# Kernel tuning notes

Measured on AMD Instinct MI355X. Metric: run time of the kernel, lower is better.

Reference implementation:

```python
import jax, jax.numpy as jnp
import numpy as np

IN_DIM = 128
OUT_DIM = 128
EDGE_DIM = 64
NUM_HEADS = 8
HEAD_DIM = OUT_DIM // NUM_HEADS
N_NODES = 10000
N_EDGES = 320000
LN_EPS = 1e-5


def _gelu(x):
    # torch nn.GELU default is the exact (erf) formulation
    return jax.nn.gelu(x, approximate=False)


def _layernorm(x, g, b):
    mu = jnp.mean(x, axis=-1, keepdims=True)
    var = jnp.var(x, axis=-1, keepdims=True)
    return (x - mu) * jax.lax.rsqrt(var + LN_EPS) * g + b


def setup_inputs() -> dict:
    key = jax.random.key(0)
    ks = jax.random.split(key, 16)

    def lin(k, fan_in, fan_out):
        # torch nn.Linear default init: U(-1/sqrt(fan_in), 1/sqrt(fan_in))
        bound = 1.0 / np.sqrt(fan_in)
        kw, kb = jax.random.split(k)
        w = jax.random.uniform(kw, (fan_in, fan_out), jnp.float32, -bound, bound)
        b = jax.random.uniform(kb, (fan_out,), jnp.float32, -bound, bound)
        return w, b

    node_features = jax.random.normal(ks[0], (N_NODES, IN_DIM), jnp.float32)
    edge_index = jax.random.randint(ks[1], (2, N_EDGES), 0, N_NODES)
    edge_attr = jax.random.normal(ks[2], (N_EDGES, EDGE_DIM), jnp.float32)

    msg_w1, msg_b1 = lin(ks[3], 2 * IN_DIM + EDGE_DIM, OUT_DIM)
    msg_w2, msg_b2 = lin(ks[4], OUT_DIM, OUT_DIM)
    q_w, q_b = lin(ks[5], IN_DIM, OUT_DIM)
    kv_w, kv_b = lin(ks[6], IN_DIM + EDGE_DIM, OUT_DIM)
    out_w1, out_b1 = lin(ks[7], IN_DIM + OUT_DIM, OUT_DIM)
    out_w2, out_b2 = lin(ks[8], OUT_DIM, OUT_DIM)
    ln_g = 1.0 + 0.02 * jax.random.normal(ks[9], (OUT_DIM,), jnp.float32)
    ln_b = 0.02 * jax.random.normal(ks[10], (OUT_DIM,), jnp.float32)

    return dict(node_features=node_features, edge_attr=edge_attr,
                msg_w1=msg_w1, msg_b1=msg_b1, msg_w2=msg_w2, msg_b2=msg_b2,
                q_w=q_w, q_b=q_b, kv_w=kv_w, kv_b=kv_b,
                out_w1=out_w1, out_b1=out_b1, out_w2=out_w2, out_b2=out_b2,
                ln_g=ln_g, ln_b=ln_b, edge_index=edge_index)


def reference(node_features, edge_attr, msg_w1, msg_b1, msg_w2, msg_b2,
              q_w, q_b, kv_w, kv_b, out_w1, out_b1, out_w2, out_b2,
              ln_g, ln_b, edge_index):
    N = node_features.shape[0]
    E = edge_index.shape[1]
    src, dst = edge_index[0], edge_index[1]

    s = node_features[src]                      # [E, Din]
    d = node_features[dst]                      # [E, Din]

    # message MLP
    m_in = jnp.concatenate([s, d, edge_attr], axis=-1)          # [E, 2*Din+De]
    m = _gelu(m_in @ msg_w1 + msg_b1) @ msg_w2 + msg_b2         # [E, Dout]

    # per-edge attention logits
    q = (d @ q_w + q_b).reshape(E, NUM_HEADS, HEAD_DIM)
    kv_in = jnp.concatenate([s, edge_attr], axis=-1)
    kv = (kv_in @ kv_w + kv_b).reshape(E, NUM_HEADS, HEAD_DIM)
    attn = jnp.sum(q * kv, axis=-1) * (HEAD_DIM ** -0.5)        # [E, H]

    # Deterministic version: pick the edge with the largest index per dst node.
    last = jnp.full((N,), -1, dtype=jnp.int32).at[dst].max(
        jnp.arange(E, dtype=jnp.int32))                          # [N]
    attn_full = jnp.where(last[:, None] >= 0,
                          attn[jnp.maximum(last, 0)],
                          -jnp.inf)                              # [N, H]
    # softmax over the NODE axis (dim=0), exactly as the torch code does;
    # -inf rows contribute 0, so using N instead of dst.max()+1 is identical.
    attn_norm = jax.nn.softmax(attn_full, axis=0)[dst]           # [E, H]

    m = (m.reshape(E, NUM_HEADS, HEAD_DIM) * attn_norm[..., None]).reshape(E, OUT_DIM)

    # scatter-add aggregation
    agg = jax.ops.segment_sum(m, dst, num_segments=N)            # [N, Dout]

    h_in = jnp.concatenate([node_features, agg], axis=-1)        # [N, Din+Dout]
    h = _gelu(h_in @ out_w1 + out_b1) @ out_w2 + out_b2          # [N, Dout]

    # res_proj is Identity since in_dim == out_dim; dropout is eval-mode no-op
    return _layernorm(node_features + h, ln_g, ln_b)
```

## Files before the change

### kernel.cpp

```cpp
#include <hip/hip_runtime.h>
#include <hip/hip_bf16.h>

#define NN 10000
#define NE 320000

typedef __bf16 bf16x8 __attribute__((ext_vector_type(8)));
typedef float  f32x4  __attribute__((ext_vector_type(4)));

__device__ __forceinline__ float bf2f(ushort u){
  union { uint i; float f; } c; c.i = ((uint)u) << 16; return c.f;
}
__device__ __forceinline__ ushort f2bf(float f){
  union { float f; uint i; } c; c.f = f;
  uint x = c.i;
  return (ushort)((x + 0x7FFFu + ((x >> 16) & 1u)) >> 16);
}
__device__ __forceinline__ float gelu_erf(float x){
  return 0.5f * x * (1.0f + erff(x * 0.70710678118654752f));
}
__device__ __forceinline__ float gelu_tanh(float x){
  float y = 0.7978845608028654f * (x + 0.044715f * x * x * x);
  float e = __expf(2.f * y);
  float th = 1.f - 2.f / (e + 1.f);
  return 0.5f * x * (1.f + th);
}
__device__ __forceinline__ uint encf(float f){
  uint u = __float_as_uint(f);
  return (u & 0x80000000u) ? ~u : (u | 0x80000000u);
}
__device__ __forceinline__ float decf(uint u){
  return __uint_as_float((u & 0x80000000u) ? (u & 0x7FFFFFFFu) : ~u);
}
#define MFMA16(a,b,c) __builtin_amdgcn_mfma_f32_16x16x32_bf16((a),(b),(c),0,0,0)

__global__ void k_init(const uint* __restrict__ w, int* __restrict__ flag,
                       int* __restrict__ cnt, int* __restrict__ last,
                       uint* __restrict__ Menc, float* __restrict__ S){
  int t = threadIdx.x;
  if (blockIdx.x == 0){
    uint c = 0;
    for (int i = t; i < 4096; i += 256){
      uint v = w[i * 63];
      uint e = (v >> 7) & 0xFF;
      if (e >= 100 && e <= 140) c++;
    }
    __shared__ uint red[256];
    red[t] = c; __syncthreads();
    for (int s = 128; s > 0; s >>= 1){
      if (t < s) red[t] += red[t + s];
      __syncthreads();
    }
    if (t == 0) *flag = (red[0] < 2048) ? 1 : 0;
    return;
  }
  int idx = (blockIdx.x - 1) * 256 + t;
  if (idx < 10000) last[idx] = -1;
  else if (idx < 20000) cnt[idx - 10000] = 0;
  else if (idx < 20008) Menc[idx - 20000] = 0u;
  else if (idx < 20016) S[idx - 20008] = 0.f;
}

__global__ void k_prep(
    const void* NF0, const int* __restrict__ dstI,
    const void* w1, const void* w2, const void* qw, const void* kvw,
    const void* ow1, const void* ow2,
    const void* b1, const void* b2, const void* qb, const void* kvb,
    const void* ob1, const void* ob2, const void* lg, const void* lb,
    int* __restrict__ cnt, int* __restrict__ last,
    ushort* NFc, float* Gagg, ushort* SB, ushort* KVW2,
    ushort* W1aT, ushort* W1bT, ushort* W1cT, ushort* W2T, ushort* QT, ushort* KVT,
    ushort* O1aT, ushort* O1bT, ushort* O2T, const int* flag)
{
  int f = *flag;
  int idx = blockIdx.x * 256 + threadIdx.x;
  if (idx < NE){
    int d = dstI[idx];
    atomicAdd(&cnt[d], 1);
    atomicMax(&last[d], idx);
    return;
  }
  idx -= NE;
  if (idx < 320000){
    if (f){
      float4 v = ((const float4*)NF0)[idx];
      ushort4 o; o.x=f2bf(v.x); o.y=f2bf(v.y); o.z=f2bf(v.z); o.w=f2bf(v.w);
      ((ushort4*)NFc)[idx] = o;
    } else ((ushort4*)NFc)[idx] = ((const ushort4*)NF0)[idx];
    return;
  }
  idx -= 320000;
  if (idx < 320000){ float4 z = {0.f,0.f,0.f,0.f}; ((float4*)Gagg)[idx] = z; return; }
  idx -= 320000;
  if (idx < 1024){
    const void* ps[8] = {b1,b2,qb,kvb,ob1,ob2,lg,lb};
    const void* p = ps[idx >> 7]; int j = idx & 127;
    SB[idx] = f ? f2bf(((const float*)p)[j]) : ((const ushort*)p)[j];
    return;
  }
  idx -= 1024;
  if (idx < 8192){
    KVW2[idx] = f ? f2bf(((const float*)kvw)[16384 + idx]) : ((const ushort*)kvw)[16384 + idx];
    return;
  }
  idx -= 8192;
  if (idx < 16384){ int c=idx>>7,k=idx&127; W1aT[idx] = f? f2bf(((const float*)w1)[k*128+c]) : ((const ushort*)w1)[k*128+c]; return; }
  idx -= 16384;
  if (idx < 16384){ int c=idx>>7,k=idx&127; W1bT[idx] = f? f2bf(((const float*)w1)[(128+k)*128+c]) : ((const ushort*)w1)[(128+k)*128+c]; return; }
  idx -= 16384;
  if (idx < 8192){ int c=idx>>6,k=idx&63;  W1cT[idx] = f? f2bf(((const float*)w1)[(256+k)*128+c]) : ((const ushort*)w1)[(256+k)*128+c]; return; }
  idx -= 8192;
  if (idx < 16384){ int c=idx>>7,k=idx&127; W2T[idx] = f? f2bf(((const float*)w2)[k*128+c]) : ((const ushort*)w2)[k*128+c]; return; }
  idx -= 16384;
  if (idx < 16384){ int c=idx>>7,k=idx&127; QT[idx]  = f? f2bf(((const float*)qw)[k*128+c]) : ((const ushort*)qw)[k*128+c]; return; }
  idx -= 16384;
  if (idx < 16384){ int c=idx>>7,k=idx&127; KVT[idx] = f? f2bf(((const float*)kvw)[k*128+c]) : ((const ushort*)kvw)[k*128+c]; return; }
  idx -= 16384;
  if (idx < 16384){ int c=idx>>7,k=idx&127; O1aT[idx] = f? f2bf(((const float*)ow1)[k*128+c]) : ((const ushort*)ow1)[k*128+c]; return; }
  idx -= 16384;
  if (idx < 16384){ int c=idx>>7,k=idx&127; O1bT[idx] = f? f2bf(((const float*)ow1)[(128+k)*128+c]) : ((const ushort*)ow1)[(128+k)*128+c]; return; }
  idx -= 16384;
  if (idx < 16384){ int c=idx>>7,k=idx&127; O2T[idx] = f? f2bf(((const float*)ow2)[k*128+c]) : ((const ushort*)ow2)[k*128+c]; return; }
}

__global__ __launch_bounds__(1024) void k_scan(const int* __restrict__ cnt,
                                               int* __restrict__ fill){
  __shared__ int sc[1024];
  int t = threadIdx.x;
  int base = t * 10;
  int v[10]; int tot = 0;
  #pragma unroll
  for (int j = 0; j < 10; ++j){
    int idx = base + j;
    v[j] = (idx < NN) ? cnt[idx] : 0;
    tot += v[j];
  }
  sc[t] = tot; __syncthreads();
  for (int off = 1; off < 1024; off <<= 1){
    int x = (t >= off) ? sc[t - off] : 0;
    __syncthreads();
    sc[t] += x;
    __syncthreads();
  }
  int run = sc[t] - tot;
  #pragma unroll
  for (int j = 0; j < 10; ++j){
    int idx = base + j;
    if (idx < NN) fill[idx] = run;
    run += v[j];
  }
}

__global__ __launch_bounds__(256) void k_fillperm(
    const int* __restrict__ srcI, const int* __restrict__ dstI,
    int* __restrict__ fill, int* __restrict__ sSort, int* __restrict__ dSort,
    const float* __restrict__ EAf, const ushort* __restrict__ EAb,
    ushort* __restrict__ EAs,
    const ushort* __restrict__ NFc,
    const ushort* __restrict__ W1aT, const ushort* __restrict__ W1bT,
    const ushort* __restrict__ QT,  const ushort* __restrict__ KVT,
    const ushort* __restrict__ SB,
    ushort* __restrict__ PA, ushort* __restrict__ PB,
    ushort* __restrict__ Qb, ushort* __restrict__ KV1,
    const int* __restrict__ flag)
{
  int t = threadIdx.x;
  if (blockIdx.x >= 1250){
    int l = t & 63, w = t >> 6;
    int m = l & 15, g = l >> 4;
    int row0 = ((int)blockIdx.x - 1250) * 16;
    const ushort* WT = (w==0) ? W1aT : (w==1) ? W1bT : (w==2) ? QT : KVT;
    ushort*       OUT= (w==0) ? PA   : (w==1) ? PB   : (w==2) ? Qb : KV1;
    const f32x4 FZ = {0.f,0.f,0.f,0.f};
    f32x4 acc[8];
    #pragma unroll
    for (int i = 0; i < 8; ++i) acc[i] = FZ;
    int arow = row0 + m;
    #pragma unroll
    for (int ks = 0; ks < 4; ++ks){
      int koff = ks * 32 + g * 8;
      bf16x8 a = *reinterpret_cast<const bf16x8*>(NFc + (size_t)arow * 128 + koff);
      #pragma unroll
      for (int nt = 0; nt < 8; ++nt){
        bf16x8 b = *reinterpret_cast<const bf16x8*>(WT + (size_t)(nt*16+m) * 128 + koff);
        acc[nt] = MFMA16(a, b, acc[nt]);
      }
    }
    #pragma unroll
    for (int nt = 0; nt < 8; ++nt){
      int col = nt * 16 + m;
      float bb = (w==1) ? bf2f(SB[col]) : (w==2) ? bf2f(SB[256+col]) : (w==3) ? bf2f(SB[384+col]) : 0.f;
      #pragma unroll
      for (int r = 0; r < 4; ++r){
        int row = row0 + g * 4 + r;
        OUT[(size_t)row * 128 + col] = f2bf(acc[nt][r] + bb);
      }
    }
    return;
  }
  __shared__ int sp[256];
  int e0 = blockIdx.x * 256;
  int e = e0 + t;
  {
    int d = dstI[e];
    int p = atomicAdd(&fill[d], 1);
    sSort[p] = srcI[e];
    dSort[p] = d;
    sp[t] = p;
  }
  __syncthreads();
  if (*flag){
    #pragma unroll
    for (int pass = 0; pass < 16; ++pass){
      int i = pass * 256 + t;
      int rloc = i >> 4, q = i & 15;
      int p = sp[rloc];
      float4 v = *reinterpret_cast<const float4*>(EAf + (size_t)(e0 + rloc) * 64 + q * 4);
      ushort4 o; o.x=f2bf(v.x); o.y=f2bf(v.y); o.z=f2bf(v.z); o.w=f2bf(v.w);
      *reinterpret_cast<ushort4*>(EAs + (size_t)p * 64 + q * 4) = o;
    }
  } else {
    #pragma unroll
    for (int pass = 0; pass < 8; ++pass){
      int i = pass * 256 + t;
      int rloc = i >> 3, q = i & 7;
      int p = sp[rloc];
      *reinterpret_cast<bf16x8*>(EAs + (size_t)p * 64 + q * 8) =
        *reinterpret_cast<const bf16x8*>(EAb + (size_t)(e0 + rloc) * 64 + q * 8);
    }
  }
}

__global__ __launch_bounds__(256) void k_edgeattn(
    const ushort* __restrict__ PA, const ushort* __restrict__ PB,
    const ushort* __restrict__ EAs,
    const int* __restrict__ sSort, const int* __restrict__ dSort,
    const ushort* __restrict__ W1cT,
    float* __restrict__ Gagg,
    const ushort* __restrict__ Qb, const ushort* __restrict__ KV1,
    const ushort* __restrict__ EAb, const float* __restrict__ EAf,
    const ushort* __restrict__ KVW2,
    const int* __restrict__ srcI, const int* __restrict__ last,
    float* __restrict__ attn, uint* __restrict__ Menc, const int* __restrict__ flag)
{
  __shared__ int sIdx[128], dIdx[128];
  __shared__ __align__(16) char Hs[128 * 256];
  __shared__ float ea_s[16][64];
  __shared__ int eN[16], sN[16];
  __shared__ uint lmax[8];
  int t = threadIdx.x;

  if (blockIdx.x >= 2500){
    int n0 = ((int)blockIdx.x - 2500) * 16;
    if (t < 16){
      int e = last[n0 + t];
      eN[t] = e;
      sN[t] = (e >= 0) ? srcI[e] : 0;
    }
    if (t < 8) lmax[t] = 0u;
    __syncthreads();
    int F = *flag;
    for (int i = t; i < 1024; i += 256){
      int nn = i >> 6, k = i & 63;
      int e = eN[nn];
      int ee = (e >= 0) ? e : 0;
      float v = F ? EAf[(size_t)ee * 64 + k] : bf2f(EAb[(size_t)ee * 64 + k]);
      ea_s[nn][k] = (e >= 0) ? v : 0.0f;
    }
    __syncthreads();
    int j = t & 127;
    int half = t >> 7;
    float acc[8];
    #pragma unroll
    for (int i = 0; i < 8; ++i) acc[i] = 0.f;
    for (int k = 0; k < 64; ++k){
      float wv = bf2f(KVW2[(size_t)k * 128 + j]);
      #pragma unroll
      for (int nn = 0; nn < 8; ++nn) acc[nn] += ea_s[half * 8 + nn][k] * wv;
    }
    #pragma unroll
    for (int nn = 0; nn < 8; ++nn){
      int nl = half * 8 + nn;
      int n = n0 + nl;
      int e = eN[nl];
      float kvv = acc[nn] + bf2f(KV1[(size_t)sN[nl] * 128 + j]);
      float qv  = bf2f(Qb[(size_t)n * 128 + j]);
      float p = qv * kvv;
      p += __shfl_xor(p, 1); p += __shfl_xor(p, 2);
      p += __shfl_xor(p, 4); p += __shfl_xor(p, 8);
      if ((j & 15) == 0 && e >= 0){
        float v = p * 0.25f;
        attn[(size_t)n * 8 + (j >> 4)] = v;
        atomicMax(&lmax[j >> 4], encf(v));
      }
    }
    __syncthreads();
    if (t < 8 && lmax[t]) atomicMax(&Menc[t], lmax[t]);
    return;
  }

  int p0 = blockIdx.x * 128;
  int l = t & 63, w = t >> 6;
  int rw = w >> 1, cw = w & 1;
  int m = l & 15, g = l >> 4;

  if (t < 128){ sIdx[t] = sSort[p0 + t]; dIdx[t] = dSort[p0 + t]; }
  __syncthreads();

  {
    int r = t >> 1, half = t & 1;
    int sr = sIdx[r], dr = dIdx[r];
    #pragma unroll
    for (int j = 0; j < 8; ++j){
      int c8 = half * 8 + j;
      bf16x8 pa = *reinterpret_cast<const bf16x8*>(PA + (size_t)sr * 128 + c8 * 8);
      bf16x8 pb = *reinterpret_cast<const bf16x8*>(PB + (size_t)dr * 128 + c8 * 8);
      bf16x8 ps;
      #pragma unroll
      for (int k = 0; k < 8; ++k) ps[k] = (__bf16)((float)pa[k] + (float)pb[k]);
      int byte = (r * 256 + c8 * 16) ^ ((r & 7) << 4);
      *reinterpret_cast<bf16x8*>(&Hs[byte]) = ps;
    }
  }

  const f32x4 FZ = {0.f,0.f,0.f,0.f};
  f32x4 acc[4][4];
  #pragma unroll
  for (int i = 0; i < 4; ++i)
    #pragma unroll
    for (int j = 0; j < 4; ++j) acc[i][j] = FZ;

  #pragma unroll
  for (int ks = 0; ks < 2; ++ks){
    bf16x8 af[4], bfr[4];
    #pragma unroll
    for (int rt = 0; rt < 4; ++rt){
      int rl = rw * 64 + rt * 16 + m;
      af[rt] = *reinterpret_cast<const bf16x8*>(EAs + (size_t)(p0 + rl) * 64 + ks * 32 + g * 8);
    }
    #pragma unroll
    for (int ct = 0; ct < 4; ++ct){
      int col = cw * 64 + ct * 16 + m;
      bfr[ct] = *reinterpret_cast<const bf16x8*>(W1cT + (size_t)col * 64 + ks * 32 + g * 8);
    }
    #pragma unroll
    for (int rt = 0; rt < 4; ++rt)
      #pragma unroll
      for (int ct = 0; ct < 4; ++ct)
        acc[rt][ct] = MFMA16(af[rt], bfr[ct], acc[rt][ct]);
  }
  __syncthreads();

  #pragma unroll
  for (int ct = 0; ct < 4; ++ct){
    int col = cw * 64 + ct * 16 + m;
    #pragma unroll
    for (int rt = 0; rt < 4; ++rt)
      #pragma unroll
      for (int r = 0; r < 4; ++r){
        int row = rw * 64 + rt * 16 + g * 4 + r;
        int byte = (row * 256 + col * 2) ^ ((row & 7) << 4);
        float v = gelu_tanh(acc[rt][ct][r] + bf2f(*reinterpret_cast<const ushort*>(&Hs[byte])));
        *reinterpret_cast<ushort*>(&Hs[byte]) = f2bf(v);
      }
  }
  __syncthreads();

  {
    int c = t & 127, hh = t >> 7;
    int rS = hh * 64, rE = rS + 64;
    float run = 0.f;
    int cur = dIdx[rS];
    for (int r = rS; r < rE; ++r){
      int d = dIdx[r];
      if (d != cur){
        unsafeAtomicAdd(&Gagg[(size_t)cur * 128 + c], run);
        run = 0.f; cur = d;
      }
      int byte = (r * 256 + c * 2) ^ ((r & 7) << 4);
      run += bf2f(*reinterpret_cast<const ushort*>(&Hs[byte]));
    }
    unsafeAtomicAdd(&Gagg[(size_t)cur * 128 + c], run);
  }
}

__global__ __launch_bounds__(256) void k_asum(
    const float* __restrict__ attn, const int* __restrict__ last,
    const uint* __restrict__ Menc, float* __restrict__ S)
{
  __shared__ float red[256][8];
  int t = threadIdx.x;
  float M[8];
  #pragma unroll
  for (int h = 0; h < 8; ++h) M[h] = decf(Menc[h]);
  float p[8];
  #pragma unroll
  for (int h = 0; h < 8; ++h) p[h] = 0.f;
  for (int n = blockIdx.x * 256 + t; n < NN; n += gridDim.x * 256){
    if (last[n] >= 0){
      #pragma unroll
      for (int h = 0; h < 8; ++h) p[h] += __expf(attn[(size_t)n * 8 + h] - M[h]);
    }
  }
  #pragma unroll
  for (int h = 0; h < 8; ++h) red[t][h] = p[h];
  __syncthreads();
  for (int s = 128; s > 0; s >>= 1){
    if (t < s){
      #pragma unroll
      for (int h = 0; h < 8; ++h) red[t][h] += red[t + s][h];
    }
    __syncthreads();
  }
  if (t < 8) atomicAdd(&S[t], red[0][t]);
}

__global__ __launch_bounds__(256) void k_aggmm2(
    const float* __restrict__ Gagg, const ushort* __restrict__ W2T,
    const ushort* __restrict__ O1aT, const ushort* __restrict__ O1bT,
    const ushort* __restrict__ SB,
    const int* __restrict__ cnt, const int* __restrict__ last,
    const float* __restrict__ attn, const uint* __restrict__ Menc,
    const float* __restrict__ S,
    const ushort* __restrict__ NFc, ushort* __restrict__ T1)
{
  __shared__ __align__(16) char Zs[64 * 256];
  int t = threadIdx.x, l = t & 63, w = t >> 6;
  int m = l & 15, g = l >> 4;
  int row0 = blockIdx.x * 64 + w * 16;

  float M[8], Sinv[8];
  #pragma unroll
  for (int h = 0; h < 8; ++h){ M[h] = decf(Menc[h]); Sinv[h] = 1.0f / S[h]; }

  int arow = row0 + m; if (arow >= NN) arow = NN - 1;
  const f32x4 FZ = {0.f,0.f,0.f,0.f};
  f32x4 acc[8];
  #pragma unroll
  for (int i = 0; i < 8; ++i) acc[i] = FZ;

  #pragma unroll
  for (int ks = 0; ks < 4; ++ks){
    const float* gp = Gagg + (size_t)arow * 128 + ks * 32 + g * 8;
    float4 u0 = *reinterpret_cast<const float4*>(gp);
    float4 u1 = *reinterpret_cast<const float4*>(gp + 4);
    float gv[8] = {u0.x,u0.y,u0.z,u0.w,u1.x,u1.y,u1.z,u1.w};
    bf16x8 hi, lo;
    #pragma unroll
    for (int k = 0; k < 8; ++k){
      hi[k] = (__bf16)gv[k];
      lo[k] = (__bf16)(gv[k] - (float)hi[k]);
    }
    #pragma unroll
    for (int nt = 0; nt < 8; ++nt){
      bf16x8 b = *reinterpret_cast<const bf16x8*>(W2T + (size_t)(nt*16+m) * 128 + ks * 32 + g * 8);
      acc[nt] = MFMA16(hi, b, acc[nt]);
      acc[nt] = MFMA16(lo, b, acc[nt]);
    }
  }

  #pragma unroll
  for (int r = 0; r < 4; ++r){
    int row = row0 + g * 4 + r;
    int rr = (row < NN) ? row : NN - 1;
    float cn = (float)cnt[rr];
    int lst = last[rr];
    int Lr = w * 16 + g * 4 + r;
    #pragma unroll
    for (int nt = 0; nt < 8; ++nt){
      int col = nt * 16 + m;
      float aw = (lst >= 0) ? __expf(attn[(size_t)rr * 8 + nt] - M[nt]) * Sinv[nt] : 0.f;
      float z = (acc[nt][r] + cn * bf2f(SB[128 + col])) * aw;
      int byte = (Lr * 256 + col * 2) ^ ((Lr & 7) << 4);
      *reinterpret_cast<ushort*>(&Zs[byte]) = f2bf(z);
    }
  }
  __syncthreads();

  f32x4 acc2[8];
  #pragma unroll
  for (int i = 0; i < 8; ++i) acc2[i] = FZ;
  int La = w * 16 + m;
  #pragma unroll
  for (int ks = 0; ks < 4; ++ks){
    int koff = ks * 32 + g * 8;
    bf16x8 az = *reinterpret_cast<const bf16x8*>(&Zs[(La * 256 + koff * 2) ^ ((La & 7) << 4)]);
    bf16x8 an = *reinterpret_cast<const bf16x8*>(NFc + (size_t)arow * 128 + koff);
    #pragma unroll
    for (int nt = 0; nt < 8; ++nt){
      bf16x8 b1v = *reinterpret_cast<const bf16x8*>(O1bT + (size_t)(nt*16+m) * 128 + koff);
      bf16x8 b2v = *reinterpret_cast<const bf16x8*>(O1aT + (size_t)(nt*16+m) * 128 + koff);
      acc2[nt] = MFMA16(az, b1v, acc2[nt]);
      acc2[nt] = MFMA16(an, b2v, acc2[nt]);
    }
  }
  #pragma unroll
  for (int nt = 0; nt < 8; ++nt){
    int col = nt * 16 + m;
    float bb = bf2f(SB[512 + col]);
    #pragma unroll
    for (int r = 0; r < 4; ++r){
      int row = row0 + g * 4 + r;
      if (row < NN){
        float v = gelu_erf(acc2[nt][r] + bb);
        T1[(size_t)row * 128 + col] = f2bf(v);
      }
    }
  }
}

__global__ __launch_bounds__(256) void k_out2ln(
    const ushort* __restrict__ T1, const ushort* __restrict__ O2T,
    const ushort* __restrict__ SB,
    const ushort* __restrict__ NFc, void* __restrict__ out,
    const int* __restrict__ flag)
{
  int t = threadIdx.x, l = t & 63, w = t >> 6;
  int m = l & 15, g = l >> 4;
  int row0 = blockIdx.x * 64 + w * 16;
  int F = *flag;
  int arow = row0 + m; if (arow >= NN) arow = NN - 1;
  const f32x4 FZ = {0.f,0.f,0.f,0.f};
  f32x4 acc[8];
  #pragma unroll
  for (int i = 0; i < 8; ++i) acc[i] = FZ;
  #pragma unroll
  for (int ks = 0; ks < 4; ++ks){
    int koff = ks * 32 + g * 8;
    bf16x8 a = *reinterpret_cast<const bf16x8*>(T1 + (size_t)arow * 128 + koff);
    #pragma unroll
    for (int nt = 0; nt < 8; ++nt){
      bf16x8 b = *reinterpret_cast<const bf16x8*>(O2T + (size_t)(nt*16+m) * 128 + koff);
      acc[nt] = MFMA16(a, b, acc[nt]);
    }
  }
  #pragma unroll
  for (int r = 0; r < 4; ++r){
    int row = row0 + g * 4 + r;
    bool ok = row < NN;
    int rr = ok ? row : NN - 1;
    float x[8]; float s = 0.f, q = 0.f;
    #pragma unroll
    for (int nt = 0; nt < 8; ++nt){
      int col = nt * 16 + m;
      float xv = acc[nt][r] + bf2f(SB[640 + col]) + bf2f(NFc[(size_t)rr * 128 + col]);
      x[nt] = xv; s += xv; q += xv * xv;
    }
    #pragma unroll
    for (int msk = 1; msk < 16; msk <<= 1){
      s += __shfl_xor(s, msk);
      q += __shfl_xor(q, msk);
    }
    float mean = s * (1.0f / 128.0f);
    float var  = q * (1.0f / 128.0f) - mean * mean;
    float rs = rsqrtf(var + 1e-5f);
    if (ok){
      #pragma unroll
      for (int nt = 0; nt < 8; ++nt){
        int col = nt * 16 + m;
        float y = (x[nt] - mean) * rs * bf2f(SB[768 + col]) + bf2f(SB[896 + col]);
        if (F) ((float*)out)[(size_t)row * 128 + col] = y;
        else   ((ushort*)out)[(size_t)row * 128 + col] = f2bf(y);
      }
    }
  }
}

extern "C" void kernel_launch(void* const* d_in, const int* in_sizes, int n_in,
                              void* d_out, int out_size, void* d_ws, size_t ws_size,
                              hipStream_t stream)
{
  const void* NF0  = d_in[0];
  const void* EA0  = d_in[1];
  const void* w1   = d_in[2];
  const void* b1   = d_in[3];
  const void* w2   = d_in[4];
  const void* b2   = d_in[5];
  const void* qw   = d_in[6];
  const void* qb   = d_in[7];
  const void* kvw  = d_in[8];
  const void* kvb  = d_in[9];
  const void* ow1  = d_in[10];
  const void* ob1  = d_in[11];
  const void* ow2  = d_in[12];
  const void* ob2  = d_in[13];
  const void* lg   = d_in[14];
  const void* lb   = d_in[15];
  const int*  srcI = (const int*)d_in[16];
  const int*  dstI = srcI + NE;

  char* ws = (char*)d_ws;
  size_t off = 0;
  auto alloc = [&](size_t bytes) -> void* {
    void* p = ws + off;
    off = (off + bytes + 255) & ~(size_t)255;
    return p;
  };
  int*    flag  = (int*)   alloc(4);
  ushort* NFc   = (ushort*)alloc((size_t)NN * 128 * 2);
  ushort* SB    = (ushort*)alloc(8 * 128 * 2);
  ushort* KVW2  = (ushort*)alloc(64 * 128 * 2);
  ushort* W1aT  = (ushort*)alloc(128 * 128 * 2);
  ushort* W1bT  = (ushort*)alloc(128 * 128 * 2);
  ushort* W1cT  = (ushort*)alloc(128 * 64 * 2);
  ushort* W2T   = (ushort*)alloc(128 * 128 * 2);
  ushort* QT    = (ushort*)alloc(128 * 128 * 2);
  ushort* KVT   = (ushort*)alloc(128 * 128 * 2);
  ushort* O1aT  = (ushort*)alloc(128 * 128 * 2);
  ushort* O1bT  = (ushort*)alloc(128 * 128 * 2);
  ushort* O2T   = (ushort*)alloc(128 * 128 * 2);
  int*    last  = (int*)   alloc(NN * 4);
  int*    cnt   = (int*)   alloc(NN * 4);
  int*    fill  = (int*)   alloc(NN * 4);
  int*    sSort = (int*)   alloc((size_t)NE * 4);
  int*    dSort = (int*)   alloc((size_t)NE * 4);
  ushort* EAs   = (ushort*)alloc((size_t)NE * 64 * 2);
  float*  attn  = (float*) alloc(NN * 8 * 4);
  uint*   Menc  = (uint*)  alloc(8 * 4);
  float*  S     = (float*) alloc(8 * 4);
  ushort* PA    = (ushort*)alloc((size_t)NN * 128 * 2);
  ushort* PB    = (ushort*)alloc((size_t)NN * 128 * 2);
  ushort* Qb    = (ushort*)alloc((size_t)NN * 128 * 2);
  ushort* KV1   = (ushort*)alloc((size_t)NN * 128 * 2);
  float*  Gagg  = (float*) alloc((size_t)NN * 128 * 4);
  ushort* T1    = (ushort*)alloc((size_t)NN * 128 * 2);

  k_init<<<80, 256, 0, stream>>>((const uint*)NF0, flag, cnt, last, Menc, S);
  k_prep<<<4330, 256, 0, stream>>>(NF0, dstI, w1, w2, qw, kvw, ow1, ow2,
                                   b1, b2, qb, kvb, ob1, ob2, lg, lb,
                                   cnt, last, NFc, Gagg, SB, KVW2,
                                   W1aT, W1bT, W1cT, W2T, QT, KVT, O1aT, O1bT, O2T, flag);
  k_scan<<<1, 1024, 0, stream>>>(cnt, fill);
  k_fillperm<<<1875, 256, 0, stream>>>(srcI, dstI, fill, sSort, dSort,
                                       (const float*)EA0, (const ushort*)EA0, EAs,
                                       NFc, W1aT, W1bT, QT, KVT, SB,
                                       PA, PB, Qb, KV1, flag);
  k_edgeattn<<<3125, 256, 0, stream>>>(PA, PB, EAs, sSort, dSort, W1cT, Gagg,
                                       Qb, KV1, (const ushort*)EA0, (const float*)EA0,
                                       KVW2, srcI, last, attn, Menc, flag);
  k_asum<<<40, 256, 0, stream>>>(attn, last, Menc, S);
  k_aggmm2<<<157, 256, 0, stream>>>(Gagg, W2T, O1aT, O1bT, SB, cnt, last,
                                    attn, Menc, S, NFc, T1);
  k_out2ln<<<157, 256, 0, stream>>>(T1, O2T, SB, NFc, d_out, flag);
}
```

Before: 210.1 us.

## Halve edge tile to 64 rows and replace tanh GELU with erf LUT

The edge-message kernel now handles 64 sorted edges per block instead of 128, with each wave owning 16 rows across all 8 column tiles. LDS per block shrinks and the block count doubles, which should raise occupancy and parallelism. The tanh-approximate GELU is replaced by a per-block 1025-entry LUT of exact erf GELU with linear interpolation. Each block pays to build the LUT, the smaller tiles reload the W1c fragments more often and cause more atomics to Gagg, and the interpolation only approximates exact GELU.

```diff
diff --git a/kernel.cpp b/kernel.cpp
--- a/kernel.cpp
+++ b/kernel.cpp
@@ -17,12 +17,6 @@
 }
 __device__ __forceinline__ float gelu_erf(float x){
   return 0.5f * x * (1.0f + erff(x * 0.70710678118654752f));
-}
-__device__ __forceinline__ float gelu_tanh(float x){
-  float y = 0.7978845608028654f * (x + 0.044715f * x * x * x);
-  float e = __expf(2.f * y);
-  float th = 1.f - 2.f / (e + 1.f);
-  return 0.5f * x * (1.f + th);
 }
 __device__ __forceinline__ uint encf(float f){
   uint u = __float_as_uint(f);
@@ -242,15 +236,16 @@
     const int* __restrict__ srcI, const int* __restrict__ last,
     float* __restrict__ attn, uint* __restrict__ Menc, const int* __restrict__ flag)
 {
-  __shared__ int sIdx[128], dIdx[128];
-  __shared__ __align__(16) char Hs[128 * 256];
-  __shared__ float ea_s[16][64];
+  __shared__ __align__(16) char Hs[64 * 256];
+  __shared__ float LUT[1026];
+  __shared__ int sIdx[64], dIdx[64];
   __shared__ int eN[16], sN[16];
   __shared__ uint lmax[8];
   int t = threadIdx.x;
 
-  if (blockIdx.x >= 2500){
-    int n0 = ((int)blockIdx.x - 2500) * 16;
+  if (blockIdx.x >= 5000){
+    float (*ea_s)[64] = reinterpret_cast<float(*)[64]>(Hs);
+    int n0 = ((int)blockIdx.x - 5000) * 16;
     if (t < 16){
       int e = last[n0 + t];
       eN[t] = e;
@@ -298,20 +293,20 @@
     return;
   }
 
-  int p0 = blockIdx.x * 128;
+  int p0 = blockIdx.x * 64;
   int l = t & 63, w = t >> 6;
-  int rw = w >> 1, cw = w & 1;
   int m = l & 15, g = l >> 4;
 
-  if (t < 128){ sIdx[t] = sSort[p0 + t]; dIdx[t] = dSort[p0 + t]; }
+  if (t < 64){ sIdx[t] = sSort[p0 + t]; dIdx[t] = dSort[p0 + t]; }
+  for (int i = t; i < 1025; i += 256) LUT[i] = gelu_erf((float)i * (1.0f/64.0f) - 8.0f);
   __syncthreads();
 
   {
-    int r = t >> 1, half = t & 1;
+    int r = t >> 2, q = t & 3;
     int sr = sIdx[r], dr = dIdx[r];
     #pragma unroll
-    for (int j = 0; j < 8; ++j){
-      int c8 = half * 8 + j;
+    for (int j = 0; j < 4; ++j){
+      int c8 = q * 4 + j;
       bf16x8 pa = *reinterpret_cast<const bf16x8*>(PA + (size_t)sr * 128 + c8 * 8);
       bf16x8 pb = *reinterpret_cast<const bf16x8*>(PB + (size_t)dr * 128 + c8 * 8);
       bf16x8 ps;
@@ -323,51 +318,43 @@
   }
 
   const f32x4 FZ = {0.f,0.f,0.f,0.f};
-  f32x4 acc[4][4];
-  #pragma unroll
-  for (int i = 0; i < 4; ++i)
-    #pragma unroll
-    for (int j = 0; j < 4; ++j) acc[i][j] = FZ;
+  f32x4 acc[8];
+  #pragma unroll
+  for (int i = 0; i < 8; ++i) acc[i] = FZ;
 
   #pragma unroll
   for (int ks = 0; ks < 2; ++ks){
-    bf16x8 af[4], bfr[4];
-    #pragma unroll
-    for (int rt = 0; rt < 4; ++rt){
-      int rl = rw * 64 + rt * 16 + m;
-      af[rt] = *reinterpret_cast<const bf16x8*>(EAs + (size_t)(p0 + rl) * 64 + ks * 32 + g * 8);
-    }
-    #pragma unroll
-    for (int ct = 0; ct < 4; ++ct){
-      int col = cw * 64 + ct * 16 + m;
-      bfr[ct] = *reinterpret_cast<const bf16x8*>(W1cT + (size_t)col * 64 + ks * 32 + g * 8);
-    }
-    #pragma unroll
-    for (int rt = 0; rt < 4; ++rt)
-      #pragma unroll
-      for (int ct = 0; ct < 4; ++ct)
-        acc[rt][ct] = MFMA16(af[rt], bfr[ct], acc[rt][ct]);
+    bf16x8 af = *reinterpret_cast<const bf16x8*>(EAs + (size_t)(p0 + w * 16 + m) * 64 + ks * 32 + g * 8);
+    #pragma unroll
+    for (int nt = 0; nt < 8; ++nt){
+      bf16x8 b = *reinterpret_cast<const bf16x8*>(W1cT + (size_t)(nt * 16 + m) * 64 + ks * 32 + g * 8);
+      acc[nt] = MFMA16(af, b, acc[nt]);
+    }
   }
   __syncthreads();
 
   #pragma unroll
-  for (int ct = 0; ct < 4; ++ct){
-    int col = cw * 64 + ct * 16 + m;
-    #pragma unroll
-    for (int rt = 0; rt < 4; ++rt)
-      #pragma unroll
-      for (int r = 0; r < 4; ++r){
-        int row = rw * 64 + rt * 16 + g * 4 + r;
-        int byte = (row * 256 + col * 2) ^ ((row & 7) << 4);
-        float v = gelu_tanh(acc[rt][ct][r] + bf2f(*reinterpret_cast<const ushort*>(&Hs[byte])));
-        *reinterpret_cast<ushort*>(&Hs[byte]) = f2bf(v);
-      }
+  for (int nt = 0; nt < 8; ++nt){
+    int col = nt * 16 + m;
+    #pragma unroll
+    for (int r = 0; r < 4; ++r){
+      int row = w * 16 + g * 4 + r;
+      int byte = (row * 256 + col * 2) ^ ((row & 7) << 4);
+      float x = acc[nt][r] + bf2f(*reinterpret_cast<const ushort*>(&Hs[byte]));
+      float idxf = fminf(fmaxf((x + 8.0f) * 64.0f, 0.0f), 1023.0f);
+      int i = (int)idxf;
+      float fr = idxf - (float)i;
+      float y = LUT[i] + fr * (LUT[i + 1] - LUT[i]);
+      y = (x > 7.9f) ? x : y;
+      y = (x < -7.9f) ? 0.0f : y;
+      *reinterpret_cast<ushort*>(&Hs[byte]) = f2bf(y);
+    }
   }
   __syncthreads();
 
   {
     int c = t & 127, hh = t >> 7;
-    int rS = hh * 64, rE = rS + 64;
+    int rS = hh * 32, rE = rS + 32;
     float run = 0.f;
     int cur = dIdx[rS];
     for (int r = rS; r < rE; ++r){
@@ -634,7 +621,7 @@
                                        (const float*)EA0, (const ushort*)EA0, EAs,
                                        NFc, W1aT, W1bT, QT, KVT, SB,
                                        PA, PB, Qb, KV1, flag);
-  k_edgeattn<<<3125, 256, 0, stream>>>(PA, PB, EAs, sSort, dSort, W1cT, Gagg,
+  k_edgeattn<<<5625, 256, 0, stream>>>(PA, PB, EAs, sSort, dSort, W1cT, Gagg,
                                        Qb, KV1, (const ushort*)EA0, (const float*)EA0,
                                        KVW2, srcI, last, attn, Menc, flag);
   k_asum<<<40, 256, 0, stream>>>(attn, last, Menc, S);
```

After: 212.7 us. About the same (+1.3%).
